# Kernel optimization log

Hardware: AMD Instinct MI355X
Metric: run time of the kernel (lower is better)

## Reference

```python
import jax, jax.numpy as jnp
import numpy as np

B, C, H, W = 32, 256, 64, 64
MIP, OUP = 8, 256
BN_EPS = 1e-5


def setup_inputs() -> dict:
    key = jax.random.key(0)
    ks = jax.random.split(key, 8)
    x = jax.random.normal(ks[0], (B, C, H, W), dtype=jnp.float32)
    # 1x1 conv weights stored as (out_ch, in_ch); BN in eval mode (running stats)
    w1 = jax.random.normal(ks[1], (MIP, C), dtype=jnp.float32) * 0.05
    bn_gamma = jnp.ones((MIP,), jnp.float32)
    bn_beta = jnp.zeros((MIP,), jnp.float32)
    bn_mean = jax.random.normal(ks[2], (MIP,), dtype=jnp.float32) * 0.1
    bn_var = jax.random.uniform(ks[3], (MIP,), dtype=jnp.float32) + 0.5
    wh = jax.random.normal(ks[4], (OUP, MIP), dtype=jnp.float32) * 0.1
    ww = jax.random.normal(ks[5], (OUP, MIP), dtype=jnp.float32) * 0.1
    return {"x": x, "w1": w1, "bn_gamma": bn_gamma, "bn_beta": bn_beta,
            "bn_mean": bn_mean, "bn_var": bn_var, "wh": wh, "ww": ww}


def _hswish(y):
    return y * jnp.clip(y + 3.0, 0.0, 6.0) / 6.0


def reference(x, w1, bn_gamma, bn_beta, bn_mean, bn_var, wh, ww):
    b, c, h, w = x.shape
    identity = x
    # Shift (mode='max'): pooled softmax profiles, outer product bias map
    bias_h = jax.nn.softmax(jnp.max(x, axis=3, keepdims=True), axis=2)  # (b,c,h,1)
    bias_w = jax.nn.softmax(jnp.max(x, axis=2, keepdims=True), axis=3)  # (b,c,1,w)
    xb = x + bias_h * bias_w  # outer product via broadcast == matmul((h,1),(1,w))
    # avg-pool profiles, concat along spatial axis -> (b,c,h+w,1)
    a_h = jnp.mean(xb, axis=3, keepdims=True)                 # (b,c,h,1)
    a_w = jnp.mean(xb, axis=2, keepdims=True).transpose(0, 1, 3, 2)  # (b,c,w,1)
    y = jnp.concatenate([a_h, a_w], axis=2)                   # (b,c,h+w,1)
    # 1x1 conv -> BN (eval) -> h_swish
    y = jnp.einsum('mc,bcsl->bmsl', w1, y)
    scale = (bn_gamma / jnp.sqrt(bn_var + BN_EPS)).reshape(1, -1, 1, 1)
    shift = (bn_beta - bn_mean * bn_gamma / jnp.sqrt(bn_var + BN_EPS)).reshape(1, -1, 1, 1)
    y = _hswish(y * scale + shift)
    # split, 1x1 convs, sigmoid gates
    y_h, y_w = y[:, :, :h], y[:, :, h:]
    g_h = jax.nn.sigmoid(jnp.einsum('om,bmhl->bohl', wh, y_h))               # (b,oup,h,1)
    g_w = jax.nn.sigmoid(jnp.einsum('om,bmwl->bowl', ww, y_w)).transpose(0, 1, 3, 2)  # (b,oup,1,w)
    return identity * g_w * g_h
```

## Files before the change

### kernel.cpp

```cpp
#include <hip/hip_runtime.h>
#include <math.h>

#define Bn 32
#define Cn 256
#define Hn 64
#define Wn 64
#define MIP 8
#define OUP 256
#define BN_EPS 1e-5f

typedef float vfloat4 __attribute__((ext_vector_type(4)));

__global__ __launch_bounds__(256) void stats_kernel(const float* __restrict__ x,
                                                    float* __restrict__ A) {
    const int bc = blockIdx.x;
    const float* xp = x + (size_t)bc * (Hn * Wn);
    __shared__ float tile[Hn * 65];
    __shared__ float pmax[256], psum[256];
    const int t = threadIdx.x;

#pragma unroll
    for (int k = 0; k < 4; ++k) {
        int i4  = t + 256 * k;
        int idx = i4 * 4;
        int h = idx >> 6;
        int w = idx & 63;
        float4 v = ((const float4*)xp)[i4];
        float* dst = &tile[h * 65 + w];
        dst[0] = v.x; dst[1] = v.y; dst[2] = v.z; dst[3] = v.w;
    }
    __syncthreads();

    {
        const int wv   = t >> 6;
        const int lane = t & 63;
        float m = -INFINITY, sm = 0.f;
        if ((wv & 1) == 0) {
            const int h = lane, w0 = (wv >> 1) * 32;
#pragma unroll 8
            for (int w = w0; w < w0 + 32; ++w) {
                float v = tile[h * 65 + w];
                m = fmaxf(m, v); sm += v;
            }
        } else {
            const int w = lane, h0 = (wv >> 1) * 32;
#pragma unroll 8
            for (int h = h0; h < h0 + 32; ++h) {
                float v = tile[h * 65 + w];
                m = fmaxf(m, v); sm += v;
            }
        }
        pmax[t] = m; psum[t] = sm;
    }
    __syncthreads();

    if (t < 128) {
        float red_max = fmaxf(pmax[t], pmax[t + 128]);
        float red_sum = psum[t] + psum[t + 128];
        float m = red_max;
#pragma unroll
        for (int off = 32; off > 0; off >>= 1) m = fmaxf(m, __shfl_xor(m, off));
        float e = __expf(red_max - m);
        float se = e;
#pragma unroll
        for (int off = 32; off > 0; off >>= 1) se += __shfl_xor(se, off);
        float a = (red_sum + e / se) * (1.0f / 64.0f);
        A[(size_t)bc * 128 + t] = a;
    }
}

__global__ __launch_bounds__(1024) void ymix_kernel(const float* __restrict__ A,
                                                    const float* __restrict__ w1,
                                                    const float* __restrict__ bn_gamma,
                                                    const float* __restrict__ bn_beta,
                                                    const float* __restrict__ bn_mean,
                                                    const float* __restrict__ bn_var,
                                                    float* __restrict__ yact) {
    const int b = blockIdx.x;
    const int t = threadIdx.x;
    const int s     = t & 127;
    const int chunk = t >> 7;

    const float* Ab = A + (size_t)b * Cn * 128;

    float acc[MIP];
#pragma unroll
    for (int m = 0; m < MIP; ++m) acc[m] = 0.f;

    const int c0 = chunk * 32;
    for (int c = c0; c < c0 + 32; ++c) {
        float a = Ab[(size_t)c * 128 + s];
#pragma unroll
        for (int m = 0; m < MIP; ++m)
            acc[m] += w1[m * Cn + c] * a;
    }

    __shared__ float red[7][MIP][128];
    if (chunk > 0) {
#pragma unroll
        for (int m = 0; m < MIP; ++m) red[chunk - 1][m][s] = acc[m];
    }
    __syncthreads();
    if (chunk == 0) {
#pragma unroll
        for (int m = 0; m < MIP; ++m) {
            float v = acc[m];
#pragma unroll
            for (int k = 0; k < 7; ++k) v += red[k][m][s];
            float sc = bn_gamma[m] * rsqrtf(bn_var[m] + BN_EPS);
            float sh = bn_beta[m] - bn_mean[m] * sc;
            v = v * sc + sh;
            v = v * fminf(fmaxf(v + 3.0f, 0.0f), 6.0f) * (1.0f / 6.0f);
            yact[(size_t)b * (MIP * 128) + m * 128 + s] = v;
        }
    }
}

__global__ __launch_bounds__(256) void apply_kernel(const float* __restrict__ x,
                                                    const float* __restrict__ yact,
                                                    const float* __restrict__ wh,
                                                    const float* __restrict__ ww,
                                                    float* __restrict__ out) {
    const int bc = blockIdx.x;
    const int b  = bc >> 8;
    const int c  = bc & 255;
    const float* xp = x + (size_t)bc * (Hn * Wn);
    float* op = out + (size_t)bc * (Hn * Wn);

    __shared__ float gs[128];
    const int t = threadIdx.x;
    if (t < 128) {
        const float* w2row = (t < 64) ? (wh + c * MIP) : (ww + c * MIP);
        const float* yb = yact + (size_t)b * (MIP * 128);
        float g = 0.f;
#pragma unroll
        for (int m = 0; m < MIP; ++m)
            g += w2row[m] * yb[m * 128 + t];
        gs[t] = 1.0f / (1.0f + __expf(-g));
    }
    __syncthreads();

#pragma unroll
    for (int k = 0; k < 4; ++k) {
        int i4  = t + 256 * k;
        int idx = i4 * 4;
        int h = idx >> 6;
        int w = idx & 63;
        vfloat4 v = __builtin_nontemporal_load(&((const vfloat4*)xp)[i4]);
        float gh = gs[h];
        float4 gw = *(const float4*)&gs[64 + w];
        vfloat4 r;
        r.x = v.x * gh * gw.x;
        r.y = v.y * gh * gw.y;
        r.z = v.z * gh * gw.z;
        r.w = v.w * gh * gw.w;
        __builtin_nontemporal_store(r, &((vfloat4*)op)[i4]);
    }
}

extern "C" void kernel_launch(void* const* d_in, const int* in_sizes, int n_in,
                              void* d_out, int out_size, void* d_ws, size_t ws_size,
                              hipStream_t stream) {
    const float* x        = (const float*)d_in[0];
    const float* w1       = (const float*)d_in[1];
    const float* bn_gamma = (const float*)d_in[2];
    const float* bn_beta  = (const float*)d_in[3];
    const float* bn_mean  = (const float*)d_in[4];
    const float* bn_var   = (const float*)d_in[5];
    const float* wh       = (const float*)d_in[6];
    const float* ww       = (const float*)d_in[7];
    float* out = (float*)d_out;

    float* A    = (float*)d_ws;
    float* yact = A + (size_t)Bn * Cn * 128;

    stats_kernel<<<Bn * Cn, 256, 0, stream>>>(x, A);
    ymix_kernel<<<Bn, 1024, 0, stream>>>(A, w1, bn_gamma, bn_beta, bn_mean,
                                         bn_var, yact);
    apply_kernel<<<Bn * Cn, 256, 0, stream>>>(x, yact, wh, ww, out);
}
```

Before: 268.4 us.

## Compute sigmoid gates in mid kernel and prefetch x before gate sync in apply

The second-stage 1x1 conv and sigmoid gates move from the apply kernel into the middle kernel, which now launches 8x more blocks (each block recomputes the per-batch y mix redundantly) and writes a precomputed gate table of B*C*128 floats. The apply kernel then just loads 128 gates per (b,c) and issues its x loads before the barrier, so memory latency overlaps the gate fetch. The cost is redundant recomputation of the channel reduction across 8 blocks per batch and an extra 4 MB gate write/read through workspace.

```diff
diff --git a/kernel.cpp b/kernel.cpp
--- a/kernel.cpp
+++ b/kernel.cpp
@@ -69,14 +69,17 @@
     }
 }
 
-__global__ __launch_bounds__(1024) void ymix_kernel(const float* __restrict__ A,
-                                                    const float* __restrict__ w1,
-                                                    const float* __restrict__ bn_gamma,
-                                                    const float* __restrict__ bn_beta,
-                                                    const float* __restrict__ bn_mean,
-                                                    const float* __restrict__ bn_var,
-                                                    float* __restrict__ yact) {
-    const int b = blockIdx.x;
+__global__ __launch_bounds__(1024) void gates_kernel(const float* __restrict__ A,
+                                                     const float* __restrict__ w1,
+                                                     const float* __restrict__ bn_gamma,
+                                                     const float* __restrict__ bn_beta,
+                                                     const float* __restrict__ bn_mean,
+                                                     const float* __restrict__ bn_var,
+                                                     const float* __restrict__ wh,
+                                                     const float* __restrict__ ww,
+                                                     float* __restrict__ gates) {
+    const int b = blockIdx.x >> 3;
+    const int j = blockIdx.x & 7;
     const int t = threadIdx.x;
     const int s     = t & 127;
     const int chunk = t >> 7;
@@ -88,6 +91,7 @@
     for (int m = 0; m < MIP; ++m) acc[m] = 0.f;
 
     const int c0 = chunk * 32;
+#pragma unroll 4
     for (int c = c0; c < c0 + 32; ++c) {
         float a = Ab[(size_t)c * 128 + s];
 #pragma unroll
@@ -96,6 +100,7 @@
     }
 
     __shared__ float red[7][MIP][128];
+    __shared__ float ys[MIP][128];
     if (chunk > 0) {
 #pragma unroll
         for (int m = 0; m < MIP; ++m) red[chunk - 1][m][s] = acc[m];
@@ -111,50 +116,61 @@
             float sh = bn_beta[m] - bn_mean[m] * sc;
             v = v * sc + sh;
             v = v * fminf(fmaxf(v + 3.0f, 0.0f), 6.0f) * (1.0f / 6.0f);
-            yact[(size_t)b * (MIP * 128) + m * 128 + s] = v;
+            ys[m][s] = v;
         }
+    }
+    __syncthreads();
+
+    const float* w2base = (s < 64) ? wh : ww;
+    float yv[MIP];
+#pragma unroll
+    for (int m = 0; m < MIP; ++m) yv[m] = ys[m][s];
+#pragma unroll
+    for (int ci = 0; ci < 4; ++ci) {
+        const int c = j * 32 + chunk * 4 + ci;
+        const float* w2 = w2base + c * MIP;
+        float g = 0.f;
+#pragma unroll
+        for (int m = 0; m < MIP; ++m) g += w2[m] * yv[m];
+        g = 1.0f / (1.0f + __expf(-g));
+        gates[((size_t)b * Cn + c) * 128 + s] = g;
     }
 }
 
 __global__ __launch_bounds__(256) void apply_kernel(const float* __restrict__ x,
-                                                    const float* __restrict__ yact,
-                                                    const float* __restrict__ wh,
-                                                    const float* __restrict__ ww,
+                                                    const float* __restrict__ gates,
                                                     float* __restrict__ out) {
     const int bc = blockIdx.x;
-    const int b  = bc >> 8;
-    const int c  = bc & 255;
     const float* xp = x + (size_t)bc * (Hn * Wn);
     float* op = out + (size_t)bc * (Hn * Wn);
+    const int t = threadIdx.x;
 
     __shared__ float gs[128];
-    const int t = threadIdx.x;
-    if (t < 128) {
-        const float* w2row = (t < 64) ? (wh + c * MIP) : (ww + c * MIP);
-        const float* yb = yact + (size_t)b * (MIP * 128);
-        float g = 0.f;
+
+    float gv = 0.f;
+    if (t < 128) gv = gates[(size_t)bc * 128 + t];
+
+    vfloat4 v[4];
 #pragma unroll
-        for (int m = 0; m < MIP; ++m)
-            g += w2row[m] * yb[m * 128 + t];
-        gs[t] = 1.0f / (1.0f + __expf(-g));
-    }
+    for (int k = 0; k < 4; ++k)
+        v[k] = __builtin_nontemporal_load(&((const vfloat4*)xp)[t + 256 * k]);
+
+    if (t < 128) gs[t] = gv;
     __syncthreads();
 
 #pragma unroll
     for (int k = 0; k < 4; ++k) {
-        int i4  = t + 256 * k;
-        int idx = i4 * 4;
+        int idx = (t + 256 * k) * 4;
         int h = idx >> 6;
         int w = idx & 63;
-        vfloat4 v = __builtin_nontemporal_load(&((const vfloat4*)xp)[i4]);
         float gh = gs[h];
         float4 gw = *(const float4*)&gs[64 + w];
         vfloat4 r;
-        r.x = v.x * gh * gw.x;
-        r.y = v.y * gh * gw.y;
-        r.z = v.z * gh * gw.z;
-        r.w = v.w * gh * gw.w;
-        __builtin_nontemporal_store(r, &((vfloat4*)op)[i4]);
+        r.x = v[k].x * gh * gw.x;
+        r.y = v[k].y * gh * gw.y;
+        r.z = v[k].z * gh * gw.z;
+        r.w = v[k].w * gh * gw.w;
+        __builtin_nontemporal_store(r, &((vfloat4*)op)[t + 256 * k]);
     }
 }
 
@@ -171,11 +187,11 @@
     const float* ww       = (const float*)d_in[7];
     float* out = (float*)d_out;
 
-    float* A    = (float*)d_ws;
-    float* yact = A + (size_t)Bn * Cn * 128;
+    float* A     = (float*)d_ws;
+    float* gates = A + (size_t)Bn * Cn * 128;
 
     stats_kernel<<<Bn * Cn, 256, 0, stream>>>(x, A);
-    ymix_kernel<<<Bn, 1024, 0, stream>>>(A, w1, bn_gamma, bn_beta, bn_mean,
-                                         bn_var, yact);
-    apply_kernel<<<Bn * Cn, 256, 0, stream>>>(x, yact, wh, ww, out);
+    gates_kernel<<<Bn * 8, 1024, 0, stream>>>(A, w1, bn_gamma, bn_beta, bn_mean,
+                                              bn_var, wh, ww, gates);
+    apply_kernel<<<Bn * Cn, 256, 0, stream>>>(x, gates, out);
 }
```

Result: no change. 270.9 us (+0.9%).
